# Kernel tuning notes

Measured on AMD Instinct MI355X. Metric: run time of the kernel, lower is better.

## Reference

```python
import jax, jax.numpy as jnp
from jax import lax
import numpy as np

N_SEQ, BATCH, HID = 512, 32, 1024

def setup_inputs() -> dict:
    key = jax.random.key(0)
    k1, k2, k3 = jax.random.split(key, 3)
    Y = jax.random.normal(k1, (N_SEQ, BATCH, 3 * HID), dtype=jnp.float32)
    init_c = jax.random.normal(k2, (1, BATCH, HID), dtype=jnp.float32)
    init_h = jax.random.normal(k3, (1, BATCH, HID), dtype=jnp.float32)
    return {"Y": Y, "init_c": init_c, "init_h": init_h}

def reference(Y, init_c, init_h):
    # QRNN fo-pooling: c_t = f_t * c_{t-1} + (1 - f_t) * z_t ; h_t = o_t * c_t
    # Zoneout dropout is evaluated in inference mode (identity), so F is used as-is.
    F, Z, O = jnp.split(Y, 3, axis=2)       # each [T, B, H]
    F = jax.nn.sigmoid(F)
    Z = jnp.tanh(Z)
    O = jax.nn.sigmoid(O)
    ZF = (1.0 - F) * Z

    def step(c, inp):
        f, zf, o = inp
        c = f * c + zf
        return c, c * o

    _, h = lax.scan(step, init_c[0], (F, ZF, O))  # h: [T, B, H]
    return jnp.concatenate([init_h, h], axis=0)   # [T+1, B, H]
```

## Files before the change

kernel.cpp:

```cpp
#include <hip/hip_runtime.h>


#define T_SEQ 512
#define BATCH 32
#define HID   1024
#define CH    (BATCH * HID)
#define ROWS  (BATCH * 3 * HID)

__device__ __forceinline__ float fast_sigmoid(float x) {
    float e = __builtin_amdgcn_exp2f(-1.4426950408889634f * x);
    return __builtin_amdgcn_rcpf(1.0f + e);
}

__device__ __forceinline__ float fast_tanh(float x) {
    float e = __builtin_amdgcn_exp2f(-2.8853900817779268f * x);
    float s = __builtin_amdgcn_rcpf(1.0f + e);
    return __builtin_fmaf(2.0f, s, -1.0f);
}

__global__ __launch_bounds__(64) void fo_pool_kernel(
        const float* __restrict__ Y,
        const float* __restrict__ init_c,
        const float* __restrict__ init_h,
        float* __restrict__ out) {
    const int ch = blockIdx.x * 64 + threadIdx.x;
    const int b  = ch >> 10;
    const int h  = ch & (HID - 1);
    const float* yb = Y + b * (3 * HID) + h;

    out[ch] = init_h[ch];
    float c = init_c[ch];

    constexpr int PF = 8;
    float fA[PF], zA[PF], oA[PF];
    float fB[PF], zB[PF], oB[PF];

    auto LOAD = [&](float* f, float* z, float* o, int t0) {
#pragma unroll
        for (int i = 0; i < PF; ++i) {
            const float* p = yb + (t0 + i) * ROWS;
            f[i] = p[0];
            z[i] = p[HID];
            o[i] = p[2 * HID];
        }
    };
    auto COMP = [&](float* f, float* z, float* o, int t0) {
#pragma unroll
        for (int i = 0; i < PF; ++i) {
            float ff = fast_sigmoid(f[i]);
            float tz = fast_tanh(z[i]);
            float oo = fast_sigmoid(o[i]);
            c = ff * c + (1.0f - ff) * tz;
            out[(t0 + i + 1) * CH + ch] = c * oo;
        }
    };

    LOAD(fA, zA, oA, 0);
    for (int t0 = 0; t0 < T_SEQ; t0 += 2 * PF) {
        LOAD(fB, zB, oB, t0 + PF);
        COMP(fA, zA, oA, t0);
        if (t0 + 2 * PF < T_SEQ) LOAD(fA, zA, oA, t0 + 2 * PF);
        COMP(fB, zB, oB, t0 + PF);
    }
}

extern "C" void kernel_launch(void* const* d_in, const int* in_sizes, int n_in,
                              void* d_out, int out_size, void* d_ws, size_t ws_size,
                              hipStream_t stream) {
    const float* Y      = (const float*)d_in[0];
    const float* init_c = (const float*)d_in[1];
    const float* init_h = (const float*)d_in[2];
    float* out = (float*)d_out;

    fo_pool_kernel<<<CH / 64, 64, 0, stream>>>(Y, init_c, init_h, out);
}
```

Measured before the change: 289.8 us.

## Split the recurrence scan into time chunks with a three-pass parallel scan

Replaces the single sequential-over-time kernel with a chunked linear-recurrence scan. The first pass computes each chunk's affine coefficients (product of forget gates and accumulated bias), a small combine kernel chains the chunk starting states, and a second pass recomputes each chunk's outputs from its start state. The aim is to lift the latency bound of only 512 wavefronts each walking 512 dependent steps, by giving the GPU 16x more independent work. The cost is extra traffic: the forget and z inputs are read twice, and the kernel now needs a workspace plus three launches.

```diff
diff --git a/kernel.cpp b/kernel.cpp
--- a/kernel.cpp
+++ b/kernel.cpp
@@ -6,62 +6,125 @@
 #define HID   1024
 #define CH    (BATCH * HID)
 #define ROWS  (BATCH * 3 * HID)
+#define NC    16
+#define CL    (T_SEQ / NC)
 
 __device__ __forceinline__ float fast_sigmoid(float x) {
     float e = __builtin_amdgcn_exp2f(-1.4426950408889634f * x);
     return __builtin_amdgcn_rcpf(1.0f + e);
 }
-
 __device__ __forceinline__ float fast_tanh(float x) {
     float e = __builtin_amdgcn_exp2f(-2.8853900817779268f * x);
     float s = __builtin_amdgcn_rcpf(1.0f + e);
     return __builtin_fmaf(2.0f, s, -1.0f);
 }
 
-__global__ __launch_bounds__(64) void fo_pool_kernel(
-        const float* __restrict__ Y,
-        const float* __restrict__ init_c,
-        const float* __restrict__ init_h,
-        float* __restrict__ out) {
+__global__ __launch_bounds__(64) void pass1(const float* __restrict__ Y,
+                                            float* __restrict__ wsA,
+                                            float* __restrict__ wsB) {
     const int ch = blockIdx.x * 64 + threadIdx.x;
+    const int k  = blockIdx.y;
     const int b  = ch >> 10;
     const int h  = ch & (HID - 1);
-    const float* yb = Y + b * (3 * HID) + h;
+    const float* yb = Y + b * (3 * HID) + h + (k * CL) * ROWS;
 
+    float A = 1.0f, Bc = 0.0f;
+    constexpr int PF = 8;
+    float fA[PF], zA[PF], fB[PF], zB[PF];
+
+    auto LOAD = [&](float* f, float* z, int t0) {
+#pragma unroll
+        for (int i = 0; i < PF; ++i) {
+            const float* p = yb + (t0 + i) * ROWS;
+            f[i] = p[0]; z[i] = p[HID];
+        }
+    };
+    auto COMP = [&](float* f, float* z) {
+#pragma unroll
+        for (int i = 0; i < PF; ++i) {
+            float ff = fast_sigmoid(f[i]);
+            float g  = (1.0f - ff) * fast_tanh(z[i]);
+            Bc = __builtin_fmaf(ff, Bc, g);
+            A *= ff;
+        }
+    };
+
+    LOAD(fA, zA, 0);
+    LOAD(fB, zB, PF);
+    COMP(fA, zA);
+    LOAD(fA, zA, 2 * PF);
+    COMP(fB, zB);
+    LOAD(fB, zB, 3 * PF);
+    COMP(fA, zA);
+    COMP(fB, zB);
+
+    wsA[k * CH + ch] = A;
+    wsB[k * CH + ch] = Bc;
+}
+
+__global__ __launch_bounds__(64) void combine(const float* __restrict__ wsA,
+                                              const float* __restrict__ wsB,
+                                              const float* __restrict__ init_c,
+                                              const float* __restrict__ init_h,
+                                              float* __restrict__ cstart,
+                                              float* __restrict__ out) {
+    const int ch = blockIdx.x * 64 + threadIdx.x;
     out[ch] = init_h[ch];
+
+    float Av[NC], Bv[NC];
+#pragma unroll
+    for (int k = 0; k < NC; ++k) {
+        Av[k] = wsA[k * CH + ch];
+        Bv[k] = wsB[k * CH + ch];
+    }
     float c = init_c[ch];
+#pragma unroll
+    for (int k = 0; k < NC; ++k) {
+        cstart[k * CH + ch] = c;
+        c = __builtin_fmaf(Av[k], c, Bv[k]);
+    }
+}
 
+__global__ __launch_bounds__(64) void pass2(const float* __restrict__ Y,
+                                            const float* __restrict__ cstart,
+                                            float* __restrict__ out) {
+    const int ch = blockIdx.x * 64 + threadIdx.x;
+    const int k  = blockIdx.y;
+    const int b  = ch >> 10;
+    const int h  = ch & (HID - 1);
+    const float* yb = Y + b * (3 * HID) + h + (k * CL) * ROWS;
+    float* ob = out + (k * CL + 1) * CH + ch;
+
+    float c = cstart[k * CH + ch];
     constexpr int PF = 8;
-    float fA[PF], zA[PF], oA[PF];
-    float fB[PF], zB[PF], oB[PF];
+    float fA[PF], zA[PF], oA[PF], fB[PF], zB[PF], oB[PF];
 
     auto LOAD = [&](float* f, float* z, float* o, int t0) {
 #pragma unroll
         for (int i = 0; i < PF; ++i) {
             const float* p = yb + (t0 + i) * ROWS;
-            f[i] = p[0];
-            z[i] = p[HID];
-            o[i] = p[2 * HID];
+            f[i] = p[0]; z[i] = p[HID]; o[i] = p[2 * HID];
         }
     };
     auto COMP = [&](float* f, float* z, float* o, int t0) {
 #pragma unroll
         for (int i = 0; i < PF; ++i) {
             float ff = fast_sigmoid(f[i]);
-            float tz = fast_tanh(z[i]);
+            float g  = (1.0f - ff) * fast_tanh(z[i]);
             float oo = fast_sigmoid(o[i]);
-            c = ff * c + (1.0f - ff) * tz;
-            out[(t0 + i + 1) * CH + ch] = c * oo;
+            c = __builtin_fmaf(ff, c, g);
+            ob[(t0 + i) * CH] = c * oo;
         }
     };
 
     LOAD(fA, zA, oA, 0);
-    for (int t0 = 0; t0 < T_SEQ; t0 += 2 * PF) {
-        LOAD(fB, zB, oB, t0 + PF);
-        COMP(fA, zA, oA, t0);
-        if (t0 + 2 * PF < T_SEQ) LOAD(fA, zA, oA, t0 + 2 * PF);
-        COMP(fB, zB, oB, t0 + PF);
-    }
+    LOAD(fB, zB, oB, PF);
+    COMP(fA, zA, oA, 0);
+    LOAD(fA, zA, oA, 2 * PF);
+    COMP(fB, zB, oB, PF);
+    LOAD(fB, zB, oB, 3 * PF);
+    COMP(fA, zA, oA, 2 * PF);
+    COMP(fB, zB, oB, 3 * PF);
 }
 
 extern "C" void kernel_launch(void* const* d_in, const int* in_sizes, int n_in,
@@ -72,5 +135,12 @@
     const float* init_h = (const float*)d_in[2];
     float* out = (float*)d_out;
 
-    fo_pool_kernel<<<CH / 64, 64, 0, stream>>>(Y, init_c, init_h, out);
+    float* wsA    = (float*)d_ws;
+    float* wsB    = wsA + NC * CH;
+    float* cstart = wsB + NC * CH;
+
+    dim3 grid(CH / 64, NC);
+    pass1<<<grid, 64, 0, stream>>>(Y, wsA, wsB);
+    combine<<<CH / 64, 64, 0, stream>>>(wsA, wsB, init_c, init_h, cstart, out);
+    pass2<<<grid, 64, 0, stream>>>(Y, cstart, out);
 }
```

Result: slower. 312.0 us (+7.7%).

## Split recurrence into time chunks with parallel scan across three kernels

Applied to the files above, without the earlier changes.

Replaces the single sequential-per-channel kernel with a chunked linear-recurrence scan. Pass1 computes per-chunk affine coefficients (A,B) in parallel over 32 time chunks, combine stitches chunk start states, and pass2 recomputes outputs per chunk, all using float4 loads. This is meant to expose far more parallelism than the previous 512 blocks of 64 threads. The cost is reading the F and Z inputs twice, extra workspace traffic, and two additional kernel launches.

```diff
diff --git a/kernel.cpp b/kernel.cpp
--- a/kernel.cpp
+++ b/kernel.cpp
@@ -5,62 +5,115 @@
 #define BATCH 32
 #define HID   1024
 #define CH    (BATCH * HID)
-#define ROWS  (BATCH * 3 * HID)
+#define CH4   (CH / 4)
+#define HID4  (HID / 4)
+#define ROWS4 (BATCH * 3 * HID4)
+#define NC    32
+#define CL    (T_SEQ / NC)
 
 __device__ __forceinline__ float fast_sigmoid(float x) {
     float e = __builtin_amdgcn_exp2f(-1.4426950408889634f * x);
     return __builtin_amdgcn_rcpf(1.0f + e);
 }
-
 __device__ __forceinline__ float fast_tanh(float x) {
     float e = __builtin_amdgcn_exp2f(-2.8853900817779268f * x);
     float s = __builtin_amdgcn_rcpf(1.0f + e);
     return __builtin_fmaf(2.0f, s, -1.0f);
 }
 
-__global__ __launch_bounds__(64) void fo_pool_kernel(
-        const float* __restrict__ Y,
-        const float* __restrict__ init_c,
-        const float* __restrict__ init_h,
-        float* __restrict__ out) {
-    const int ch = blockIdx.x * 64 + threadIdx.x;
-    const int b  = ch >> 10;
-    const int h  = ch & (HID - 1);
-    const float* yb = Y + b * (3 * HID) + h;
+__device__ __forceinline__ void step1(float f, float z, float& A, float& B) {
+    float ff = fast_sigmoid(f);
+    float g  = (1.0f - ff) * fast_tanh(z);
+    B = __builtin_fmaf(ff, B, g);
+    A *= ff;
+}
+__device__ __forceinline__ float step2(float f, float z, float o, float& c) {
+    float ff = fast_sigmoid(f);
+    float g  = (1.0f - ff) * fast_tanh(z);
+    c = __builtin_fmaf(ff, c, g);
+    return c * fast_sigmoid(o);
+}
 
+__global__ __launch_bounds__(256, 4) void pass1(const float4* __restrict__ Y4,
+                                                float4* __restrict__ wsA,
+                                                float4* __restrict__ wsB) {
+    const int c4 = blockIdx.x * 256 + threadIdx.x;
+    const int k  = blockIdx.y;
+    const int b  = c4 >> 8;
+    const int h4 = c4 & (HID4 - 1);
+    const float4* yb = Y4 + b * (3 * HID4) + h4 + (size_t)(k * CL) * ROWS4;
+
+    float4 A = make_float4(1.f, 1.f, 1.f, 1.f);
+    float4 B = make_float4(0.f, 0.f, 0.f, 0.f);
+
+    float4 f0 = yb[0], z0 = yb[HID4];
+#pragma unroll
+    for (int t = 0; t < CL; ++t) {
+        float4 f1, z1;
+        if (t + 1 < CL) {
+            const float4* p = yb + (size_t)(t + 1) * ROWS4;
+            f1 = p[0]; z1 = p[HID4];
+        }
+        step1(f0.x, z0.x, A.x, B.x);
+        step1(f0.y, z0.y, A.y, B.y);
+        step1(f0.z, z0.z, A.z, B.z);
+        step1(f0.w, z0.w, A.w, B.w);
+        f0 = f1; z0 = z1;
+    }
+    wsA[(size_t)k * CH4 + c4] = A;
+    wsB[(size_t)k * CH4 + c4] = B;
+}
+
+__global__ __launch_bounds__(256) void combine(const float* __restrict__ wsA,
+                                               const float* __restrict__ wsB,
+                                               const float* __restrict__ init_c,
+                                               const float* __restrict__ init_h,
+                                               float* __restrict__ cstart,
+                                               float* __restrict__ out) {
+    const int ch = blockIdx.x * 256 + threadIdx.x;
     out[ch] = init_h[ch];
+
+    float Av[NC], Bv[NC];
+#pragma unroll
+    for (int k = 0; k < NC; ++k) {
+        Av[k] = wsA[(size_t)k * CH + ch];
+        Bv[k] = wsB[(size_t)k * CH + ch];
+    }
     float c = init_c[ch];
+#pragma unroll
+    for (int k = 0; k < NC; ++k) {
+        cstart[(size_t)k * CH + ch] = c;
+        c = __builtin_fmaf(Av[k], c, Bv[k]);
+    }
+}
 
-    constexpr int PF = 8;
-    float fA[PF], zA[PF], oA[PF];
-    float fB[PF], zB[PF], oB[PF];
+__global__ __launch_bounds__(256, 4) void pass2(const float4* __restrict__ Y4,
+                                                const float4* __restrict__ cstart4,
+                                                float4* __restrict__ out4) {
+    const int c4 = blockIdx.x * 256 + threadIdx.x;
+    const int k  = blockIdx.y;
+    const int b  = c4 >> 8;
+    const int h4 = c4 & (HID4 - 1);
+    const float4* yb = Y4 + b * (3 * HID4) + h4 + (size_t)(k * CL) * ROWS4;
+    float4* ob = out4 + (size_t)(k * CL + 1) * CH4 + c4;
 
-    auto LOAD = [&](float* f, float* z, float* o, int t0) {
+    float4 c = cstart4[(size_t)k * CH4 + c4];
+
+    float4 f0 = yb[0], z0 = yb[HID4], o0 = yb[2 * HID4];
 #pragma unroll
-        for (int i = 0; i < PF; ++i) {
-            const float* p = yb + (t0 + i) * ROWS;
-            f[i] = p[0];
-            z[i] = p[HID];
-            o[i] = p[2 * HID];
+    for (int t = 0; t < CL; ++t) {
+        float4 f1, z1, o1;
+        if (t + 1 < CL) {
+            const float4* p = yb + (size_t)(t + 1) * ROWS4;
+            f1 = p[0]; z1 = p[HID4]; o1 = p[2 * HID4];
         }
-    };
-    auto COMP = [&](float* f, float* z, float* o, int t0) {
-#pragma unroll
-        for (int i = 0; i < PF; ++i) {
-            float ff = fast_sigmoid(f[i]);
-            float tz = fast_tanh(z[i]);
-            float oo = fast_sigmoid(o[i]);
-            c = ff * c + (1.0f - ff) * tz;
-            out[(t0 + i + 1) * CH + ch] = c * oo;
-        }
-    };
-
-    LOAD(fA, zA, oA, 0);
-    for (int t0 = 0; t0 < T_SEQ; t0 += 2 * PF) {
-        LOAD(fB, zB, oB, t0 + PF);
-        COMP(fA, zA, oA, t0);
-        if (t0 + 2 * PF < T_SEQ) LOAD(fA, zA, oA, t0 + 2 * PF);
-        COMP(fB, zB, oB, t0 + PF);
+        float4 hh;
+        hh.x = step2(f0.x, z0.x, o0.x, c.x);
+        hh.y = step2(f0.y, z0.y, o0.y, c.y);
+        hh.z = step2(f0.z, z0.z, o0.z, c.z);
+        hh.w = step2(f0.w, z0.w, o0.w, c.w);
+        ob[(size_t)t * CH4] = hh;
+        f0 = f1; z0 = z1; o0 = o1;
     }
 }
 
@@ -72,5 +125,12 @@
     const float* init_h = (const float*)d_in[2];
     float* out = (float*)d_out;
 
-    fo_pool_kernel<<<CH / 64, 64, 0, stream>>>(Y, init_c, init_h, out);
+    float* wsA    = (float*)d_ws;
+    float* wsB    = wsA + (size_t)NC * CH;
+    float* cstart = wsB + (size_t)NC * CH;
+
+    dim3 grid(CH4 / 256, NC);
+    pass1<<<grid, 256, 0, stream>>>((const float4*)Y, (float4*)wsA, (float4*)wsB);
+    combine<<<CH / 256, 256, 0, stream>>>(wsA, wsB, init_c, init_h, cstart, out);
+    pass2<<<grid, 256, 0, stream>>>((const float4*)Y, (const float4*)cstart, (float4*)out);
 }
```

After: 310.2 us. 7.0% more time.

## Parallelize recurrence over time chunks with block-level linear scan

Applied to the files above, without the earlier changes.

Splits the sequence into 64 time chunks per channel group, each handled by its own thread, which computes a chunk-local affine composition (A,B) of the recurrence. A single lane group then scans across chunks in shared memory to get each chunk's initial carry, after which every thread replays its chunk to emit outputs. Loads and stores now use float4. The goal is to break the serial 512-step dependency and raise memory-level parallelism, at the cost of keeping 8 float4 gate pairs per thread in registers and a serial 64-step cross-chunk scan done by 16 threads.

```diff
diff --git a/kernel.cpp b/kernel.cpp
--- a/kernel.cpp
+++ b/kernel.cpp
@@ -5,62 +5,109 @@
 #define BATCH 32
 #define HID   1024
 #define CH    (BATCH * HID)
-#define ROWS  (BATCH * 3 * HID)
+#define CH4   (CH / 4)
+#define HID4  (HID / 4)
+#define ROWS4 (BATCH * 3 * HID4)
+#define NC    64
+#define CL    (T_SEQ / NC)
+#define JW    16
+#define NTHR  (NC * JW)
 
 __device__ __forceinline__ float fast_sigmoid(float x) {
     float e = __builtin_amdgcn_exp2f(-1.4426950408889634f * x);
     return __builtin_amdgcn_rcpf(1.0f + e);
 }
-
 __device__ __forceinline__ float fast_tanh(float x) {
     float e = __builtin_amdgcn_exp2f(-2.8853900817779268f * x);
     float s = __builtin_amdgcn_rcpf(1.0f + e);
     return __builtin_fmaf(2.0f, s, -1.0f);
 }
+__device__ __forceinline__ float4 sig4(float4 v) {
+    return make_float4(fast_sigmoid(v.x), fast_sigmoid(v.y),
+                       fast_sigmoid(v.z), fast_sigmoid(v.w));
+}
+__device__ __forceinline__ float4 tanh4(float4 v) {
+    return make_float4(fast_tanh(v.x), fast_tanh(v.y),
+                       fast_tanh(v.z), fast_tanh(v.w));
+}
 
-__global__ __launch_bounds__(64) void fo_pool_kernel(
-        const float* __restrict__ Y,
-        const float* __restrict__ init_c,
-        const float* __restrict__ init_h,
-        float* __restrict__ out) {
-    const int ch = blockIdx.x * 64 + threadIdx.x;
-    const int b  = ch >> 10;
-    const int h  = ch & (HID - 1);
-    const float* yb = Y + b * (3 * HID) + h;
+__global__ __launch_bounds__(NTHR, 4) void fo_pool_fused(
+        const float4* __restrict__ Y4,
+        const float4* __restrict__ init_c4,
+        const float4* __restrict__ init_h4,
+        float4* __restrict__ out4) {
+    __shared__ float4 sA[NC][JW];
+    __shared__ float4 sB[NC][JW];
 
-    out[ch] = init_h[ch];
-    float c = init_c[ch];
+    const int tid = threadIdx.x;
+    const int k   = tid >> 4;
+    const int j   = tid & (JW - 1);
+    const int c4  = blockIdx.x * JW + j;
+    const int b   = c4 >> 8;
+    const int h4  = c4 & (HID4 - 1);
+    const float4* yb = Y4 + b * (3 * HID4) + h4 + (size_t)(k * CL) * ROWS4;
 
-    constexpr int PF = 8;
-    float fA[PF], zA[PF], oA[PF];
-    float fB[PF], zB[PF], oB[PF];
+    float4 ff[CL], gg[CL];
+    float4 A = make_float4(1.f, 1.f, 1.f, 1.f);
+    float4 B = make_float4(0.f, 0.f, 0.f, 0.f);
 
-    auto LOAD = [&](float* f, float* z, float* o, int t0) {
+    float4 f0 = yb[0], z0 = yb[HID4];
 #pragma unroll
-        for (int i = 0; i < PF; ++i) {
-            const float* p = yb + (t0 + i) * ROWS;
-            f[i] = p[0];
-            z[i] = p[HID];
-            o[i] = p[2 * HID];
+    for (int t = 0; t < CL; ++t) {
+        float4 f1, z1;
+        if (t + 1 < CL) {
+            const float4* p = yb + (size_t)(t + 1) * ROWS4;
+            f1 = p[0]; z1 = p[HID4];
         }
-    };
-    auto COMP = [&](float* f, float* z, float* o, int t0) {
+        float4 s  = sig4(f0);
+        float4 th = tanh4(z0);
+        float4 g  = make_float4((1.f - s.x) * th.x, (1.f - s.y) * th.y,
+                                (1.f - s.z) * th.z, (1.f - s.w) * th.w);
+        ff[t] = s; gg[t] = g;
+        B.x = __builtin_fmaf(s.x, B.x, g.x);
+        B.y = __builtin_fmaf(s.y, B.y, g.y);
+        B.z = __builtin_fmaf(s.z, B.z, g.z);
+        B.w = __builtin_fmaf(s.w, B.w, g.w);
+        A.x *= s.x; A.y *= s.y; A.z *= s.z; A.w *= s.w;
+        f0 = f1; z0 = z1;
+    }
+    sA[k][j] = A;
+    sB[k][j] = B;
+    __syncthreads();
+
+    if (tid < JW) {
+        const int cc4 = blockIdx.x * JW + tid;
+        out4[cc4] = init_h4[cc4];
+        float4 c = init_c4[cc4];
 #pragma unroll
-        for (int i = 0; i < PF; ++i) {
-            float ff = fast_sigmoid(f[i]);
-            float tz = fast_tanh(z[i]);
-            float oo = fast_sigmoid(o[i]);
-            c = ff * c + (1.0f - ff) * tz;
-            out[(t0 + i + 1) * CH + ch] = c * oo;
+        for (int kk = 0; kk < NC; ++kk) {
+            float4 a  = sA[kk][tid];
+            float4 b0 = sB[kk][tid];
+            sA[kk][tid] = c;
+            c.x = __builtin_fmaf(a.x, c.x, b0.x);
+            c.y = __builtin_fmaf(a.y, c.y, b0.y);
+            c.z = __builtin_fmaf(a.z, c.z, b0.z);
+            c.w = __builtin_fmaf(a.w, c.w, b0.w);
         }
-    };
+    }
+    __syncthreads();
 
-    LOAD(fA, zA, oA, 0);
-    for (int t0 = 0; t0 < T_SEQ; t0 += 2 * PF) {
-        LOAD(fB, zB, oB, t0 + PF);
-        COMP(fA, zA, oA, t0);
-        if (t0 + 2 * PF < T_SEQ) LOAD(fA, zA, oA, t0 + 2 * PF);
-        COMP(fB, zB, oB, t0 + PF);
+    float4 c = sA[k][j];
+    float4* ob = out4 + (size_t)(k * CL + 1) * CH4 + c4;
+
+    float4 o0 = yb[2 * HID4];
+#pragma unroll
+    for (int t = 0; t < CL; ++t) {
+        float4 o1;
+        if (t + 1 < CL) o1 = (yb + (size_t)(t + 1) * ROWS4)[2 * HID4];
+        c.x = __builtin_fmaf(ff[t].x, c.x, gg[t].x);
+        c.y = __builtin_fmaf(ff[t].y, c.y, gg[t].y);
+        c.z = __builtin_fmaf(ff[t].z, c.z, gg[t].z);
+        c.w = __builtin_fmaf(ff[t].w, c.w, gg[t].w);
+        float4 oo = sig4(o0);
+        float4 hh = make_float4(c.x * oo.x, c.y * oo.y, c.z * oo.z, c.w * oo.w);
+        ob[(size_t)t * CH4] = hh;
+        o0 = o1;
     }
 }
 
@@ -72,5 +119,6 @@
     const float* init_h = (const float*)d_in[2];
     float* out = (float*)d_out;
 
-    fo_pool_kernel<<<CH / 64, 64, 0, stream>>>(Y, init_c, init_h, out);
+    fo_pool_fused<<<CH4 / JW, NTHR, 0, stream>>>(
+        (const float4*)Y, (const float4*)init_c, (const float4*)init_h, (float4*)out);
 }
```

New measurement: 306.6 us. 1.06x slower.
